# Kernel optimization log

Measured on AMD Instinct MI355X. Metric: run time of the kernel, lower is better.

## Reference

```python
import jax, jax.numpy as jnp
import numpy as np

OSC_TIME = 10
UNITS = 256
D_IN = 256
BATCH = 32
SEQLEN = 2000


def setup_inputs() -> dict:
    key = jax.random.key(0)
    k1, k2, k3 = jax.random.split(key, 3)
    scale = 1.0 / np.sqrt(UNITS)
    x = jax.random.normal(k1, (BATCH, SEQLEN, D_IN), dtype=jnp.float32)
    W_x = jax.random.normal(k2, (4, 2, D_IN, UNITS), dtype=jnp.float32) * scale
    W_h = jax.random.normal(k3, (4, 2, UNITS, UNITS), dtype=jnp.float32) * scale
    b_x = jnp.zeros((4, 2, UNITS), dtype=jnp.float32)
    b_h = jnp.zeros((4, 2, UNITS), dtype=jnp.float32)
    return {"x": x, "W_x": W_x, "b_x": b_x, "W_h": W_h, "b_h": b_h}


def reference(x, W_x, b_x, W_h, b_h):
    # Subsample every OSC_TIME steps (tf.gather stride)
    xs = x[:, ::OSC_TIME]                       # [B, Ts, D]
    B, Ts, _ = xs.shape
    U = W_h.shape[-1]

    # Precompute input projections for all 4 cells x 2 gates: [4,2,B,Ts,U]
    xp = jnp.einsum('btd,cgdu->cgbtu', xs, W_x) + b_x[:, :, None, None, :]

    h0 = jnp.zeros((4, B, U), dtype=x.dtype)

    def ff_step(h, xp_t):                       # h [4,B,U], xp_t [4,2,B,U]
        hp = jnp.einsum('cbu,cguv->cgbv', h, W_h) + b_h[:, :, None, :]
        g = jax.nn.sigmoid(xp_t + hp)           # [4,2,B,U]
        j, k = g[:, 0], g[:, 1]
        h_new = j * (1.0 - h) + (1.0 - k) * h   # flip-flop update
        return h_new, h_new

    _, hs = jax.lax.scan(ff_step, h0, jnp.moveaxis(xp, 3, 0))  # hs [Ts,4,B,U]
    phi, omega, r, mu = hs[:, 0], hs[:, 1], hs[:, 2], hs[:, 3]  # each [Ts,B,U]

    # Oscillator: emit z = r*cos(phi) then update r, phi; OSC_TIME sub-steps
    def osc_step(carry, _):
        r_t, phi_t = carry
        z = r_t * jnp.cos(phi_t)
        r_n = r_t + (mu - jnp.square(r_t)) * r_t
        phi_n = phi_t + omega
        return (r_n, phi_n), z

    _, zs = jax.lax.scan(osc_step, (r, phi), None, length=OSC_TIME)  # [S,Ts,B,U]
    out = jnp.transpose(zs, (2, 1, 0, 3)).reshape(B, Ts * OSC_TIME, U)
    return out
```

## Files before the change

### kernel.cpp

```cpp
#include <hip/hip_runtime.h>
#include <hip/hip_fp16.h>
#include <stdint.h>

#define TS 200

typedef _Float16 h2_t  __attribute__((ext_vector_type(2)));
typedef _Float16 f16x8 __attribute__((ext_vector_type(8)));
typedef float    f32x4 __attribute__((ext_vector_type(4)));

static __device__ __forceinline__ float fdot2f(uint32_t w, uint32_t h, float acc) {
#if __has_builtin(__builtin_amdgcn_fdot2)
    return __builtin_amdgcn_fdot2(__builtin_bit_cast(h2_t, w),
                                  __builtin_bit_cast(h2_t, h), acc, false);
#else
    h2_t a = __builtin_bit_cast(h2_t, w), b = __builtin_bit_cast(h2_t, h);
    acc = fmaf((float)a.x, (float)b.x, acc);
    acc = fmaf((float)a.y, (float)b.y, acc);
    return acc;
#endif
}

template <int CTRL>
static __device__ __forceinline__ float dpp_add(float x) {
    int m = __builtin_amdgcn_update_dpp(0, __builtin_bit_cast(int, x), CTRL, 0xF, 0xF, true);
    return x + __builtin_bit_cast(float, m);
}
template <int CTRL>
static __device__ __forceinline__ float dpp_mov(float x) {
    int m = __builtin_amdgcn_update_dpp(0, __builtin_bit_cast(int, x), CTRL, 0xF, 0xF, true);
    return __builtin_bit_cast(float, m);
}

__global__ __launch_bounds__(256) void pack_all(const float* __restrict__ x,
                                                const float* __restrict__ Wx,
                                                const float* __restrict__ Wh,
                                                _Float16* __restrict__ xh,
                                                _Float16* __restrict__ wxt,
                                                uint32_t* __restrict__ wp) {
    int bid = blockIdx.x, tid = threadIdx.x;
    if (bid < 6400) {
        int row = bid, col = tid;
        int b = row / 200, t = row - b * 200;
        xh[(size_t)row * 256 + col] = (_Float16)x[((size_t)(b * 2000 + t * 10)) * 256 + col];
    } else if (bid < 8448) {
        int n = bid - 6400, k = tid;
        wxt[(size_t)n * 256 + k] = (_Float16)Wx[((size_t)((n >> 8) * 256 + k)) * 256 + (n & 255)];
    } else {
        int idx = (bid - 8448) * 256 + tid;
        int e   = idx & 3;
        int thr = (idx >> 2) & 1023;
        int j   = (idx >> 12) & 15;
        int c   = idx >> 16;
        int a = j >> 2, i = j & 3;
        int uu = a >> 1, g = a & 1;
        int vs = thr & 7, uq = (thr >> 3) & 7, wv = thr >> 6;
        int u = (wv * 8 + uq) * 2 + uu;
        int v = vs * 32 + i * 8 + e * 2;
        const float* base = Wh + ((size_t)((c * 2 + g) * 256 + v)) * 256 + u;
        h2_t p; p.x = (_Float16)base[0]; p.y = (_Float16)base[256];
        wp[idx] = __builtin_bit_cast(uint32_t, p);
    }
}

__global__ __launch_bounds__(256) void xp_gemm(const _Float16* __restrict__ xh,
                                               const _Float16* __restrict__ wxt,
                                               const float* __restrict__ bxf,
                                               _Float16* __restrict__ xp) {
    __shared__ _Float16 As[128 * 64];
    __shared__ _Float16 Bs[128 * 64];
    const int tid = threadIdx.x;
    const int lane = tid & 63, w = tid >> 6;
    const int m0 = (blockIdx.x >> 4) * 128;
    const int n0 = (blockIdx.x & 15) * 128;
    const int mw = (w & 1) * 64, nw = (w >> 1) * 64;

    f32x4 acc[4][4] = {};

    for (int kb = 0; kb < 4; kb++) {
        const int k0 = kb * 64;
#pragma unroll
        for (int q = 0; q < 4; q++) {
            int ii = w * 4 + q;
            int r = ii * 8 + (lane >> 3);
            int kcol = (lane & 7) * 8;
            const _Float16* ga = xh  + (size_t)(m0 + r) * 256 + k0 + kcol;
            const _Float16* gb = wxt + (size_t)(n0 + r) * 256 + k0 + kcol;
            __builtin_amdgcn_global_load_lds(
                (const __attribute__((address_space(1))) uint32_t*)ga,
                (__attribute__((address_space(3))) uint32_t*)(As + ii * 512), 16, 0, 0);
            __builtin_amdgcn_global_load_lds(
                (const __attribute__((address_space(1))) uint32_t*)gb,
                (__attribute__((address_space(3))) uint32_t*)(Bs + ii * 512), 16, 0, 0);
        }
        __syncthreads();
#pragma unroll
        for (int kc = 0; kc < 2; kc++) {
            f16x8 a[4], b[4];
#pragma unroll
            for (int mt = 0; mt < 4; mt++)
                a[mt] = *(const f16x8*)&As[(mw + mt * 16 + (lane & 15)) * 64 + kc * 32 + (lane >> 4) * 8];
#pragma unroll
            for (int nt = 0; nt < 4; nt++)
                b[nt] = *(const f16x8*)&Bs[(nw + nt * 16 + (lane & 15)) * 64 + kc * 32 + (lane >> 4) * 8];
#pragma unroll
            for (int mt = 0; mt < 4; mt++)
#pragma unroll
                for (int nt = 0; nt < 4; nt++)
                    acc[mt][nt] = __builtin_amdgcn_mfma_f32_16x16x32_f16(a[mt], b[nt], acc[mt][nt], 0, 0, 0);
        }
        __syncthreads();
    }

    const int nl = lane & 15, quad = lane >> 4;
#pragma unroll
    for (int nt = 0; nt < 4; nt++) {
        int n = n0 + nw + nt * 16 + nl;
        float bias = bxf[n];
        int c = n >> 9, gu = n & 511;
#pragma unroll
        for (int mt = 0; mt < 4; mt++)
#pragma unroll
            for (int r = 0; r < 4; r++) {
                int m = m0 + mw + mt * 16 + quad * 4 + r;
                int b = m / 200, t = m - b * 200;
                xp[((size_t)((c * 32 + b) * 200 + t)) * 512 + gu] =
                    (_Float16)(acc[mt][nt][r] + bias);
            }
    }
}

#define D4(ACC, W, H)                 \
    ACC = fdot2f(W.x, H.x, ACC);      \
    ACC = fdot2f(W.y, H.y, ACC);      \
    ACC = fdot2f(W.z, H.z, ACC);      \
    ACC = fdot2f(W.w, H.w, ACC);

#define PIN4(W) asm volatile("" : "+v"(W.x), "+v"(W.y), "+v"(W.z), "+v"(W.w))

__global__ __attribute__((amdgpu_flat_work_group_size(512, 512),
                          amdgpu_waves_per_eu(2, 2)))
void recurrence(const _Float16* __restrict__ xp,
                const float* __restrict__ bh,
                const uint32_t* __restrict__ Wp,
                float* __restrict__ hs) {
    const int cb  = blockIdx.x;
    const int c   = cb >> 5;
    const int tid = threadIdx.x;
    const int lane = tid & 63;
    const int vs = lane & 7;
    const int uq = lane >> 3;
    const int wv = tid >> 6;
    const int up0 = wv * 8 + uq;
    const int u0 = up0 * 2;

    __shared__ __align__(16) uint32_t h2s[2][160];

    const uint4* wb = (const uint4*)Wp + (size_t)c * 16 * 1024 + tid;
    uint4 wA00 = wb[0 * 1024],        wA01 = wb[1 * 1024],        wA02 = wb[2 * 1024],        wA03 = wb[3 * 1024];
    uint4 wA10 = wb[4 * 1024],        wA11 = wb[5 * 1024],        wA12 = wb[6 * 1024],        wA13 = wb[7 * 1024];
    uint4 wA20 = wb[8 * 1024],        wA21 = wb[9 * 1024],        wA22 = wb[10 * 1024],       wA23 = wb[11 * 1024];
    uint4 wA30 = wb[12 * 1024],       wA31 = wb[13 * 1024],       wA32 = wb[14 * 1024],       wA33 = wb[15 * 1024];
    uint4 wB00 = wb[0 * 1024 + 512],  wB01 = wb[1 * 1024 + 512],  wB02 = wb[2 * 1024 + 512],  wB03 = wb[3 * 1024 + 512];
    uint4 wB10 = wb[4 * 1024 + 512],  wB11 = wb[5 * 1024 + 512],  wB12 = wb[6 * 1024 + 512],  wB13 = wb[7 * 1024 + 512];
    uint4 wB20 = wb[8 * 1024 + 512],  wB21 = wb[9 * 1024 + 512],  wB22 = wb[10 * 1024 + 512], wB23 = wb[11 * 1024 + 512];
    uint4 wB30 = wb[12 * 1024 + 512], wB31 = wb[13 * 1024 + 512], wB32 = wb[14 * 1024 + 512], wB33 = wb[15 * 1024 + 512];
    PIN4(wA00); PIN4(wA01); PIN4(wA02); PIN4(wA03);
    PIN4(wA10); PIN4(wA11); PIN4(wA12); PIN4(wA13);
    PIN4(wA20); PIN4(wA21); PIN4(wA22); PIN4(wA23);
    PIN4(wA30); PIN4(wA31); PIN4(wA32); PIN4(wA33);
    PIN4(wB00); PIN4(wB01); PIN4(wB02); PIN4(wB03);
    PIN4(wB10); PIN4(wB11); PIN4(wB12); PIN4(wB13);
    PIN4(wB20); PIN4(wB21); PIN4(wB22); PIN4(wB23);
    PIN4(wB30); PIN4(wB31); PIN4(wB32); PIN4(wB33);

    float biasA = 0.f, biasB = 0.f;
    const _Float16* xpb = nullptr;
    if (vs < 4) {
        int g_sel = vs & 1, u_sel = u0 + (vs >> 1);
        biasA = bh[(c * 2 + g_sel) * 256 + u_sel];
        biasB = bh[(c * 2 + g_sel) * 256 + u_sel + 128];
        xpb  = xp + (size_t)cb * 200 * 512 + g_sel * 256 + u_sel;
    }

    float hregA = 0.f, hregB = 0.f;
    if (tid < 160) { h2s[0][tid] = 0u; }
    __syncthreads();

    float* hsb = hs + (size_t)cb * 200 * 256 + u0;

    for (int t = 0; t < TS; t++) {
        const uint32_t* hbuf = h2s[t & 1];
        uint32_t* hnext = h2s[(t + 1) & 1];

        float xpA = 0.f, xpB = 0.f;
        if (vs < 4) {
            xpA = (float)xpb[(size_t)t * 512];
            xpB = (float)xpb[(size_t)t * 512 + 128];
        }

        uint4 h0 = *(const uint4*)(hbuf + vs * 20 + 0);
        uint4 h1 = *(const uint4*)(hbuf + vs * 20 + 4);
        uint4 h2 = *(const uint4*)(hbuf + vs * 20 + 8);
        uint4 h3 = *(const uint4*)(hbuf + vs * 20 + 12);

        float aA0 = 0.f, aA1 = 0.f, aA2 = 0.f, aA3 = 0.f;
        float aB0 = 0.f, aB1 = 0.f, aB2 = 0.f, aB3 = 0.f;
        D4(aA0, wA00, h0) D4(aB0, wB00, h0) D4(aA1, wA10, h0) D4(aB1, wB10, h0)
        D4(aA2, wA20, h0) D4(aB2, wB20, h0) D4(aA3, wA30, h0) D4(aB3, wB30, h0)
        D4(aA0, wA01, h1) D4(aB0, wB01, h1) D4(aA1, wA11, h1) D4(aB1, wB11, h1)
        D4(aA2, wA21, h1) D4(aB2, wB21, h1) D4(aA3, wA31, h1) D4(aB3, wB31, h1)
        D4(aA0, wA02, h2) D4(aB0, wB02, h2) D4(aA1, wA12, h2) D4(aB1, wB12, h2)
        D4(aA2, wA22, h2) D4(aB2, wB22, h2) D4(aA3, wA32, h2) D4(aB3, wB32, h2)
        D4(aA0, wA03, h3) D4(aB0, wB03, h3) D4(aA1, wA13, h3) D4(aB1, wB13, h3)
        D4(aA2, wA23, h3) D4(aB2, wB23, h3) D4(aA3, wA33, h3) D4(aB3, wB33, h3)

        aA0 = dpp_add<0x141>(dpp_add<0x4E>(dpp_add<0xB1>(aA0)));
        aA1 = dpp_add<0x141>(dpp_add<0x4E>(dpp_add<0xB1>(aA1)));
        aA2 = dpp_add<0x141>(dpp_add<0x4E>(dpp_add<0xB1>(aA2)));
        aA3 = dpp_add<0x141>(dpp_add<0x4E>(dpp_add<0xB1>(aA3)));
        aB0 = dpp_add<0x141>(dpp_add<0x4E>(dpp_add<0xB1>(aB0)));
        aB1 = dpp_add<0x141>(dpp_add<0x4E>(dpp_add<0xB1>(aB1)));
        aB2 = dpp_add<0x141>(dpp_add<0x4E>(dpp_add<0xB1>(aB2)));
        aB3 = dpp_add<0x141>(dpp_add<0x4E>(dpp_add<0xB1>(aB3)));

        float sA = (vs == 0) ? aA0 : (vs == 1) ? aA1 : (vs == 2) ? aA2 : aA3;
        float sB = (vs == 0) ? aB0 : (vs == 1) ? aB1 : (vs == 2) ? aB2 : aB3;
        sA += xpA + biasA;
        sB += xpB + biasB;
        float sigA = 1.f / (1.f + __expf(-sA));
        float sigB = 1.f / (1.f + __expf(-sB));
        float kgA = dpp_mov<0xB1>(sigA);
        float kgB = dpp_mov<0xB1>(sigB);
        float hnA = sigA + hregA * (1.f - sigA - kgA);
        float hnB = sigB + hregB * (1.f - sigB - kgB);
        hregA = hnA;
        hregB = hnB;
        float hn1A = dpp_mov<0x4E>(hnA);
        float hn1B = dpp_mov<0x4E>(hnB);
        if (vs == 0) {
            h2_t pA; pA.x = (_Float16)hnA; pA.y = (_Float16)hn1A;
            h2_t pB; pB.x = (_Float16)hnB; pB.y = (_Float16)hn1B;
            int idx0 = (up0 >> 4) * 20 + (up0 & 15);
            hnext[idx0]      = __builtin_bit_cast(uint32_t, pA);
            hnext[idx0 + 80] = __builtin_bit_cast(uint32_t, pB);
            *(float2*)(hsb + (size_t)t * 256)       = make_float2(hnA, hn1A);
            *(float2*)(hsb + (size_t)t * 256 + 128) = make_float2(hnB, hn1B);
        }
        __syncthreads();
    }
}

__global__ __launch_bounds__(256) void osc(const float* __restrict__ hs,
                                           float* __restrict__ out) {
    int tid = blockIdx.x * 256 + threadIdx.x;
    const int cstride = 32 * 200 * 256;
    int u = tid & 255;
    int bt = tid >> 8;
    int t = bt % 200, b = bt / 200;
    float phi   = hs[0 * cstride + tid];
    float omega = hs[1 * cstride + tid];
    float r     = hs[2 * cstride + tid];
    float mu    = hs[3 * cstride + tid];
    float* o = out + ((size_t)(b * 2000 + t * 10)) * 256 + u;
#pragma unroll
    for (int s = 0; s < 10; s++) {
        o[(size_t)s * 256] = r * __cosf(phi);
        r = r + (mu - r * r) * r;
        phi = phi + omega;
    }
}

extern "C" void kernel_launch(void* const* d_in, const int* in_sizes, int n_in,
                              void* d_out, int out_size, void* d_ws, size_t ws_size,
                              hipStream_t stream) {
    const float* x  = (const float*)d_in[0];
    const float* Wx = (const float*)d_in[1];
    const float* bx = (const float*)d_in[2];
    const float* Wh = (const float*)d_in[3];
    const float* bh = (const float*)d_in[4];
    float* out = (float*)d_out;

    char* ws = (char*)d_ws;
    const size_t XP = (size_t)4 * 32 * 200 * 512 * 2;
    const size_t HS = (size_t)4 * 32 * 200 * 256 * 4;
    const size_t XH = (size_t)6400 * 256 * 2;

    _Float16* xp  = (_Float16*)ws;
    float*    hs  = (float*)(ws + XP);
    _Float16* xh  = (_Float16*)(ws + XP);
    _Float16* wxt = (_Float16*)(ws + XP + XH);
    uint32_t* wp  = (uint32_t*)(ws + XP + HS);

    pack_all<<<9472, 256, 0, stream>>>(x, Wx, Wh, xh, wxt, wp);
    xp_gemm<<<800, 256, 0, stream>>>(xh, wxt, bx, xp);
    recurrence<<<128, 512, 0, stream>>>(xp, bh, wp, hs);
    osc<<<6400, 256, 0, stream>>>(hs, out);
}
```

Baseline: 381.2 us.

## Prefetch xp projections eight steps ahead and use LDS-only barrier in recurrence

The recurrence loop is blocked by 8 timesteps, and the xp input projections for the next block are loaded into registers while the current block runs. This takes global-memory latency off the serial per-step critical path. __syncthreads is replaced by a barrier that waits only on LDS counters (lgkmcnt), so the per-step barrier no longer waits for outstanding global loads and stores. The cost is more register pressure from the prefetch buffers, under a tight waves_per_eu(2,2) budget that holds many pinned weights.

```diff
diff --git a/kernel.cpp b/kernel.cpp
--- a/kernel.cpp
+++ b/kernel.cpp
@@ -137,6 +137,14 @@
 
 #define PIN4(W) asm volatile("" : "+v"(W.x), "+v"(W.y), "+v"(W.z), "+v"(W.w))
 
+#define LDS_BARRIER()                                        \
+    do {                                                     \
+        __builtin_amdgcn_sched_barrier(0);                   \
+        asm volatile("s_waitcnt lgkmcnt(0)" ::: "memory");   \
+        __builtin_amdgcn_s_barrier();                        \
+        __builtin_amdgcn_sched_barrier(0);                   \
+    } while (0)
+
 __global__ __attribute__((amdgpu_flat_work_group_size(512, 512),
                           amdgpu_waves_per_eu(2, 2)))
 void recurrence(const _Float16* __restrict__ xp,
@@ -188,65 +196,89 @@
 
     float* hsb = hs + (size_t)cb * 200 * 256 + u0;
 
-    for (int t = 0; t < TS; t++) {
-        const uint32_t* hbuf = h2s[t & 1];
-        uint32_t* hnext = h2s[(t + 1) & 1];
-
-        float xpA = 0.f, xpB = 0.f;
+    _Float16 curA[8] = {}, curB[8] = {}, nxtA[8] = {}, nxtB[8] = {};
+    if (vs < 4) {
+#pragma unroll
+        for (int s = 0; s < 8; s++) {
+            curA[s] = xpb[(size_t)s * 512];
+            curB[s] = xpb[(size_t)s * 512 + 128];
+        }
+    }
+
+    for (int tb = 0; tb < TS; tb += 8) {
+        if (vs < 4 && tb + 8 < TS) {
+#pragma unroll
+            for (int s = 0; s < 8; s++) {
+                nxtA[s] = xpb[(size_t)(tb + 8 + s) * 512];
+                nxtB[s] = xpb[(size_t)(tb + 8 + s) * 512 + 128];
+            }
+        }
+#pragma unroll
+        for (int s = 0; s < 8; s++) {
+            const int t = tb + s;
+            const uint32_t* hbuf = h2s[t & 1];
+            uint32_t* hnext = h2s[(t + 1) & 1];
+
+            float xpA = 0.f, xpB = 0.f;
+            if (vs < 4) {
+                xpA = (float)curA[s];
+                xpB = (float)curB[s];
+            }
+
+            uint4 h0 = *(const uint4*)(hbuf + vs * 20 + 0);
+            uint4 h1 = *(const uint4*)(hbuf + vs * 20 + 4);
+            uint4 h2 = *(const uint4*)(hbuf + vs * 20 + 8);
+            uint4 h3 = *(const uint4*)(hbuf + vs * 20 + 12);
+
+            float aA0 = 0.f, aA1 = 0.f, aA2 = 0.f, aA3 = 0.f;
+            float aB0 = 0.f, aB1 = 0.f, aB2 = 0.f, aB3 = 0.f;
+            D4(aA0, wA00, h0) D4(aB0, wB00, h0) D4(aA1, wA10, h0) D4(aB1, wB10, h0)
+            D4(aA2, wA20, h0) D4(aB2, wB20, h0) D4(aA3, wA30, h0) D4(aB3, wB30, h0)
+            D4(aA0, wA01, h1) D4(aB0, wB01, h1) D4(aA1, wA11, h1) D4(aB1, wB11, h1)
+            D4(aA2, wA21, h1) D4(aB2, wB21, h1) D4(aA3, wA31, h1) D4(aB3, wB31, h1)
+            D4(aA0, wA02, h2) D4(aB0, wB02, h2) D4(aA1, wA12, h2) D4(aB1, wB12, h2)
+            D4(aA2, wA22, h2) D4(aB2, wB22, h2) D4(aA3, wA32, h2) D4(aB3, wB32, h2)
+            D4(aA0, wA03, h3) D4(aB0, wB03, h3) D4(aA1, wA13, h3) D4(aB1, wB13, h3)
+            D4(aA2, wA23, h3) D4(aB2, wB23, h3) D4(aA3, wA33, h3) D4(aB3, wB33, h3)
+
+            aA0 = dpp_add<0x141>(dpp_add<0x4E>(dpp_add<0xB1>(aA0)));
+            aA1 = dpp_add<0x141>(dpp_add<0x4E>(dpp_add<0xB1>(aA1)));
+            aA2 = dpp_add<0x141>(dpp_add<0x4E>(dpp_add<0xB1>(aA2)));
+            aA3 = dpp_add<0x141>(dpp_add<0x4E>(dpp_add<0xB1>(aA3)));
+            aB0 = dpp_add<0x141>(dpp_add<0x4E>(dpp_add<0xB1>(aB0)));
+            aB1 = dpp_add<0x141>(dpp_add<0x4E>(dpp_add<0xB1>(aB1)));
+            aB2 = dpp_add<0x141>(dpp_add<0x4E>(dpp_add<0xB1>(aB2)));
+            aB3 = dpp_add<0x141>(dpp_add<0x4E>(dpp_add<0xB1>(aB3)));
+
+            float sA = (vs == 0) ? aA0 : (vs == 1) ? aA1 : (vs == 2) ? aA2 : aA3;
+            float sB = (vs == 0) ? aB0 : (vs == 1) ? aB1 : (vs == 2) ? aB2 : aB3;
+            sA += xpA + biasA;
+            sB += xpB + biasB;
+            float sigA = 1.f / (1.f + __expf(-sA));
+            float sigB = 1.f / (1.f + __expf(-sB));
+            float kgA = dpp_mov<0xB1>(sigA);
+            float kgB = dpp_mov<0xB1>(sigB);
+            float hnA = sigA + hregA * (1.f - sigA - kgA);
+            float hnB = sigB + hregB * (1.f - sigB - kgB);
+            hregA = hnA;
+            hregB = hnB;
+            float hn1A = dpp_mov<0x4E>(hnA);
+            float hn1B = dpp_mov<0x4E>(hnB);
+            if (vs == 0) {
+                h2_t pA; pA.x = (_Float16)hnA; pA.y = (_Float16)hn1A;
+                h2_t pB; pB.x = (_Float16)hnB; pB.y = (_Float16)hn1B;
+                int idx0 = (up0 >> 4) * 20 + (up0 & 15);
+                hnext[idx0]      = __builtin_bit_cast(uint32_t, pA);
+                hnext[idx0 + 80] = __builtin_bit_cast(uint32_t, pB);
+                *(float2*)(hsb + (size_t)t * 256)       = make_float2(hnA, hn1A);
+                *(float2*)(hsb + (size_t)t * 256 + 128) = make_float2(hnB, hn1B);
+            }
+            LDS_BARRIER();
+        }
         if (vs < 4) {
-            xpA = (float)xpb[(size_t)t * 512];
-            xpB = (float)xpb[(size_t)t * 512 + 128];
-        }
-
-        uint4 h0 = *(const uint4*)(hbuf + vs * 20 + 0);
-        uint4 h1 = *(const uint4*)(hbuf + vs * 20 + 4);
-        uint4 h2 = *(const uint4*)(hbuf + vs * 20 + 8);
-        uint4 h3 = *(const uint4*)(hbuf + vs * 20 + 12);
-
-        float aA0 = 0.f, aA1 = 0.f, aA2 = 0.f, aA3 = 0.f;
-        float aB0 = 0.f, aB1 = 0.f, aB2 = 0.f, aB3 = 0.f;
-        D4(aA0, wA00, h0) D4(aB0, wB00, h0) D4(aA1, wA10, h0) D4(aB1, wB10, h0)
-        D4(aA2, wA20, h0) D4(aB2, wB20, h0) D4(aA3, wA30, h0) D4(aB3, wB30, h0)
-        D4(aA0, wA01, h1) D4(aB0, wB01, h1) D4(aA1, wA11, h1) D4(aB1, wB11, h1)
-        D4(aA2, wA21, h1) D4(aB2, wB21, h1) D4(aA3, wA31, h1) D4(aB3, wB31, h1)
-        D4(aA0, wA02, h2) D4(aB0, wB02, h2) D4(aA1, wA12, h2) D4(aB1, wB12, h2)
-        D4(aA2, wA22, h2) D4(aB2, wB22, h2) D4(aA3, wA32, h2) D4(aB3, wB32, h2)
-        D4(aA0, wA03, h3) D4(aB0, wB03, h3) D4(aA1, wA13, h3) D4(aB1, wB13, h3)
-        D4(aA2, wA23, h3) D4(aB2, wB23, h3) D4(aA3, wA33, h3) D4(aB3, wB33, h3)
-
-        aA0 = dpp_add<0x141>(dpp_add<0x4E>(dpp_add<0xB1>(aA0)));
-        aA1 = dpp_add<0x141>(dpp_add<0x4E>(dpp_add<0xB1>(aA1)));
-        aA2 = dpp_add<0x141>(dpp_add<0x4E>(dpp_add<0xB1>(aA2)));
-        aA3 = dpp_add<0x141>(dpp_add<0x4E>(dpp_add<0xB1>(aA3)));
-        aB0 = dpp_add<0x141>(dpp_add<0x4E>(dpp_add<0xB1>(aB0)));
-        aB1 = dpp_add<0x141>(dpp_add<0x4E>(dpp_add<0xB1>(aB1)));
-        aB2 = dpp_add<0x141>(dpp_add<0x4E>(dpp_add<0xB1>(aB2)));
-        aB3 = dpp_add<0x141>(dpp_add<0x4E>(dpp_add<0xB1>(aB3)));
-
-        float sA = (vs == 0) ? aA0 : (vs == 1) ? aA1 : (vs == 2) ? aA2 : aA3;
-        float sB = (vs == 0) ? aB0 : (vs == 1) ? aB1 : (vs == 2) ? aB2 : aB3;
-        sA += xpA + biasA;
-        sB += xpB + biasB;
-        float sigA = 1.f / (1.f + __expf(-sA));
-        float sigB = 1.f / (1.f + __expf(-sB));
-        float kgA = dpp_mov<0xB1>(sigA);
-        float kgB = dpp_mov<0xB1>(sigB);
-        float hnA = sigA + hregA * (1.f - sigA - kgA);
-        float hnB = sigB + hregB * (1.f - sigB - kgB);
-        hregA = hnA;
-        hregB = hnB;
-        float hn1A = dpp_mov<0x4E>(hnA);
-        float hn1B = dpp_mov<0x4E>(hnB);
-        if (vs == 0) {
-            h2_t pA; pA.x = (_Float16)hnA; pA.y = (_Float16)hn1A;
-            h2_t pB; pB.x = (_Float16)hnB; pB.y = (_Float16)hn1B;
-            int idx0 = (up0 >> 4) * 20 + (up0 & 15);
-            hnext[idx0]      = __builtin_bit_cast(uint32_t, pA);
-            hnext[idx0 + 80] = __builtin_bit_cast(uint32_t, pB);
-            *(float2*)(hsb + (size_t)t * 256)       = make_float2(hnA, hn1A);
-            *(float2*)(hsb + (size_t)t * 256 + 128) = make_float2(hnB, hn1B);
-        }
-        __syncthreads();
+#pragma unroll
+            for (int s = 0; s < 8; s++) { curA[s] = nxtA[s]; curB[s] = nxtB[s]; }
+        }
     }
 }
 
```

Result: faster. 344.9 us (-9.5%).

## Process two batch rows per workgroup in recurrence with prefetched xp and lighter barrier

Applied to the files above, without the earlier changes.

Each recurrence workgroup now advances two independent batch sequences, sharing the register-resident W_h weights, so the grid shrinks from 128 to 64 blocks. Interleaving two independent dot-product chains is meant to hide the latency of each serial step and of the per-step barrier. The xp input for step t+1 is prefetched during step t, and __syncthreads is replaced by an LDS-only wait plus s_barrier so outstanding global loads and stores need not drain. The costs are roughly double the per-step work per block, higher register pressure, and half as many CUs in use.

```diff
diff --git a/kernel.cpp b/kernel.cpp
--- a/kernel.cpp
+++ b/kernel.cpp
@@ -137,14 +137,27 @@
 
 #define PIN4(W) asm volatile("" : "+v"(W.x), "+v"(W.y), "+v"(W.z), "+v"(W.w))
 
+#define RED3(A) A = dpp_add<0x141>(dpp_add<0x4E>(dpp_add<0xB1>(A)));
+
+#define LDS_BARRIER()                                        \
+    do {                                                     \
+        __builtin_amdgcn_sched_barrier(0);                   \
+        asm volatile("s_waitcnt lgkmcnt(0)" ::: "memory");   \
+        __builtin_amdgcn_s_barrier();                        \
+        __builtin_amdgcn_sched_barrier(0);                   \
+    } while (0)
+
 __global__ __attribute__((amdgpu_flat_work_group_size(512, 512),
                           amdgpu_waves_per_eu(2, 2)))
 void recurrence(const _Float16* __restrict__ xp,
                 const float* __restrict__ bh,
                 const uint32_t* __restrict__ Wp,
                 float* __restrict__ hs) {
-    const int cb  = blockIdx.x;
-    const int c   = cb >> 5;
+    const int wg  = blockIdx.x;
+    const int c   = wg >> 4;
+    const int b0  = wg & 15;
+    const int cbP = c * 32 + b0;
+    const int cbQ = cbP + 16;
     const int tid = threadIdx.x;
     const int lane = tid & 63;
     const int vs = lane & 7;
@@ -153,7 +166,8 @@
     const int up0 = wv * 8 + uq;
     const int u0 = up0 * 2;
 
-    __shared__ __align__(16) uint32_t h2s[2][160];
+    __shared__ __align__(16) uint32_t h2sP[2][160];
+    __shared__ __align__(16) uint32_t h2sQ[2][160];
 
     const uint4* wb = (const uint4*)Wp + (size_t)c * 16 * 1024 + tid;
     uint4 wA00 = wb[0 * 1024],        wA01 = wb[1 * 1024],        wA02 = wb[2 * 1024],        wA03 = wb[3 * 1024];
@@ -174,79 +188,123 @@
     PIN4(wB30); PIN4(wB31); PIN4(wB32); PIN4(wB33);
 
     float biasA = 0.f, biasB = 0.f;
-    const _Float16* xpb = nullptr;
+    const _Float16* xpbP = nullptr;
+    const _Float16* xpbQ = nullptr;
     if (vs < 4) {
         int g_sel = vs & 1, u_sel = u0 + (vs >> 1);
         biasA = bh[(c * 2 + g_sel) * 256 + u_sel];
         biasB = bh[(c * 2 + g_sel) * 256 + u_sel + 128];
-        xpb  = xp + (size_t)cb * 200 * 512 + g_sel * 256 + u_sel;
-    }
-
-    float hregA = 0.f, hregB = 0.f;
-    if (tid < 160) { h2s[0][tid] = 0u; }
+        xpbP = xp + (size_t)cbP * 200 * 512 + g_sel * 256 + u_sel;
+        xpbQ = xp + (size_t)cbQ * 200 * 512 + g_sel * 256 + u_sel;
+    }
+
+    float hrAP = 0.f, hrBP = 0.f;
+    float hrAQ = 0.f, hrBQ = 0.f;
+    if (tid < 160) { h2sP[0][tid] = 0u; h2sQ[0][tid] = 0u; }
     __syncthreads();
 
-    float* hsb = hs + (size_t)cb * 200 * 256 + u0;
+    float* hsbP = hs + (size_t)cbP * 200 * 256 + u0;
+    float* hsbQ = hs + (size_t)cbQ * 200 * 256 + u0;
+
+    float cAP = 0.f, cBP = 0.f, cAQ = 0.f, cBQ = 0.f;
+    _Float16 nAP = (_Float16)0.f, nBP = (_Float16)0.f;
+    _Float16 nAQ = (_Float16)0.f, nBQ = (_Float16)0.f;
+    if (vs < 4) {
+        cAP = (float)xpbP[0]; cBP = (float)xpbP[128];
+        cAQ = (float)xpbQ[0]; cBQ = (float)xpbQ[128];
+    }
 
     for (int t = 0; t < TS; t++) {
-        const uint32_t* hbuf = h2s[t & 1];
-        uint32_t* hnext = h2s[(t + 1) & 1];
-
-        float xpA = 0.f, xpB = 0.f;
+        const uint32_t* hbP = h2sP[t & 1];
+        uint32_t* hnP = h2sP[(t + 1) & 1];
+        const uint32_t* hbQ = h2sQ[t & 1];
+        uint32_t* hnQ = h2sQ[(t + 1) & 1];
+
+        if (vs < 4 && t + 1 < TS) {
+            nAP = xpbP[(size_t)(t + 1) * 512];
+            nBP = xpbP[(size_t)(t + 1) * 512 + 128];
+            nAQ = xpbQ[(size_t)(t + 1) * 512];
+            nBQ = xpbQ[(size_t)(t + 1) * 512 + 128];
+        }
+
+        uint4 hP0 = *(const uint4*)(hbP + vs * 20 + 0);
+        uint4 hP1 = *(const uint4*)(hbP + vs * 20 + 4);
+        uint4 hP2 = *(const uint4*)(hbP + vs * 20 + 8);
+        uint4 hP3 = *(const uint4*)(hbP + vs * 20 + 12);
+        uint4 hQ0 = *(const uint4*)(hbQ + vs * 20 + 0);
+        uint4 hQ1 = *(const uint4*)(hbQ + vs * 20 + 4);
+        uint4 hQ2 = *(const uint4*)(hbQ + vs * 20 + 8);
+        uint4 hQ3 = *(const uint4*)(hbQ + vs * 20 + 12);
+
+        float aAP0 = 0.f, aAP1 = 0.f, aAP2 = 0.f, aAP3 = 0.f;
+        float aBP0 = 0.f, aBP1 = 0.f, aBP2 = 0.f, aBP3 = 0.f;
+        float aAQ0 = 0.f, aAQ1 = 0.f, aAQ2 = 0.f, aAQ3 = 0.f;
+        float aBQ0 = 0.f, aBQ1 = 0.f, aBQ2 = 0.f, aBQ3 = 0.f;
+        D4(aAP0, wA00, hP0) D4(aAQ0, wA00, hQ0) D4(aBP0, wB00, hP0) D4(aBQ0, wB00, hQ0)
+        D4(aAP1, wA10, hP0) D4(aAQ1, wA10, hQ0) D4(aBP1, wB10, hP0) D4(aBQ1, wB10, hQ0)
+        D4(aAP2, wA20, hP0) D4(aAQ2, wA20, hQ0) D4(aBP2, wB20, hP0) D4(aBQ2, wB20, hQ0)
+        D4(aAP3, wA30, hP0) D4(aAQ3, wA30, hQ0) D4(aBP3, wB30, hP0) D4(aBQ3, wB30, hQ0)
+        D4(aAP0, wA01, hP1) D4(aAQ0, wA01, hQ1) D4(aBP0, wB01, hP1) D4(aBQ0, wB01, hQ1)
+        D4(aAP1, wA11, hP1) D4(aAQ1, wA11, hQ1) D4(aBP1, wB11, hP1) D4(aBQ1, wB11, hQ1)
+        D4(aAP2, wA21, hP1) D4(aAQ2, wA21, hQ1) D4(aBP2, wB21, hP1) D4(aBQ2, wB21, hQ1)
+        D4(aAP3, wA31, hP1) D4(aAQ3, wA31, hQ1) D4(aBP3, wB31, hP1) D4(aBQ3, wB31, hQ1)
+        D4(aAP0, wA02, hP2) D4(aAQ0, wA02, hQ2) D4(aBP0, wB02, hP2) D4(aBQ0, wB02, hQ2)
+        D4(aAP1, wA12, hP2) D4(aAQ1, wA12, hQ2) D4(aBP1, wB12, hP2) D4(aBQ1, wB12, hQ2)
+        D4(aAP2, wA22, hP2) D4(aAQ2, wA22, hQ2) D4(aBP2, wB22, hP2) D4(aBQ2, wB22, hQ2)
+        D4(aAP3, wA32, hP2) D4(aAQ3, wA32, hQ2) D4(aBP3, wB32, hP2) D4(aBQ3, wB32, hQ2)
+        D4(aAP0, wA03, hP3) D4(aAQ0, wA03, hQ3) D4(aBP0, wB03, hP3) D4(aBQ0, wB03, hQ3)
+        D4(aAP1, wA13, hP3) D4(aAQ1, wA13, hQ3) D4(aBP1, wB13, hP3) D4(aBQ1, wB13, hQ3)
+        D4(aAP2, wA23, hP3) D4(aAQ2, wA23, hQ3) D4(aBP2, wB23, hP3) D4(aBQ2, wB23, hQ3)
+        D4(aAP3, wA33, hP3) D4(aAQ3, wA33, hQ3) D4(aBP3, wB33, hP3) D4(aBQ3, wB33, hQ3)
+
+        RED3(aAP0) RED3(aAP1) RED3(aAP2) RED3(aAP3)
+        RED3(aBP0) RED3(aBP1) RED3(aBP2) RED3(aBP3)
+        RED3(aAQ0) RED3(aAQ1) RED3(aAQ2) RED3(aAQ3)
+        RED3(aBQ0) RED3(aBQ1) RED3(aBQ2) RED3(aBQ3)
+
+        float sAP = (vs == 0) ? aAP0 : (vs == 1) ? aAP1 : (vs == 2) ? aAP2 : aAP3;
+        float sBP = (vs == 0) ? aBP0 : (vs == 1) ? aBP1 : (vs == 2) ? aBP2 : aBP3;
+        float sAQ = (vs == 0) ? aAQ0 : (vs == 1) ? aAQ1 : (vs == 2) ? aAQ2 : aAQ3;
+        float sBQ = (vs == 0) ? aBQ0 : (vs == 1) ? aBQ1 : (vs == 2) ? aBQ2 : aBQ3;
+        sAP += cAP + biasA;  sBP += cBP + biasB;
+        sAQ += cAQ + biasA;  sBQ += cBQ + biasB;
+        float gAP = 1.f / (1.f + __expf(-sAP));
+        float gBP = 1.f / (1.f + __expf(-sBP));
+        float gAQ = 1.f / (1.f + __expf(-sAQ));
+        float gBQ = 1.f / (1.f + __expf(-sBQ));
+        float kAP = dpp_mov<0xB1>(gAP);
+        float kBP = dpp_mov<0xB1>(gBP);
+        float kAQ = dpp_mov<0xB1>(gAQ);
+        float kBQ = dpp_mov<0xB1>(gBQ);
+        float hnAP = gAP + hrAP * (1.f - gAP - kAP);
+        float hnBP = gBP + hrBP * (1.f - gBP - kBP);
+        float hnAQ = gAQ + hrAQ * (1.f - gAQ - kAQ);
+        float hnBQ = gBQ + hrBQ * (1.f - gBQ - kBQ);
+        hrAP = hnAP; hrBP = hnBP; hrAQ = hnAQ; hrBQ = hnBQ;
+        float h1AP = dpp_mov<0x4E>(hnAP);
+        float h1BP = dpp_mov<0x4E>(hnBP);
+        float h1AQ = dpp_mov<0x4E>(hnAQ);
+        float h1BQ = dpp_mov<0x4E>(hnBQ);
+        if (vs == 0) {
+            h2_t pAP; pAP.x = (_Float16)hnAP; pAP.y = (_Float16)h1AP;
+            h2_t pBP; pBP.x = (_Float16)hnBP; pBP.y = (_Float16)h1BP;
+            h2_t pAQ; pAQ.x = (_Float16)hnAQ; pAQ.y = (_Float16)h1AQ;
+            h2_t pBQ; pBQ.x = (_Float16)hnBQ; pBQ.y = (_Float16)h1BQ;
+            int idx0 = (up0 >> 4) * 20 + (up0 & 15);
+            hnP[idx0]      = __builtin_bit_cast(uint32_t, pAP);
+            hnP[idx0 + 80] = __builtin_bit_cast(uint32_t, pBP);
+            hnQ[idx0]      = __builtin_bit_cast(uint32_t, pAQ);
+            hnQ[idx0 + 80] = __builtin_bit_cast(uint32_t, pBQ);
+            *(float2*)(hsbP + (size_t)t * 256)       = make_float2(hnAP, h1AP);
+            *(float2*)(hsbP + (size_t)t * 256 + 128) = make_float2(hnBP, h1BP);
+            *(float2*)(hsbQ + (size_t)t * 256)       = make_float2(hnAQ, h1AQ);
+            *(float2*)(hsbQ + (size_t)t * 256 + 128) = make_float2(hnBQ, h1BQ);
+        }
+        LDS_BARRIER();
         if (vs < 4) {
-            xpA = (float)xpb[(size_t)t * 512];
-            xpB = (float)xpb[(size_t)t * 512 + 128];
-        }
-
-        uint4 h0 = *(const uint4*)(hbuf + vs * 20 + 0);
-        uint4 h1 = *(const uint4*)(hbuf + vs * 20 + 4);
-        uint4 h2 = *(const uint4*)(hbuf + vs * 20 + 8);
-        uint4 h3 = *(const uint4*)(hbuf + vs * 20 + 12);
-
-        float aA0 = 0.f, aA1 = 0.f, aA2 = 0.f, aA3 = 0.f;
-        float aB0 = 0.f, aB1 = 0.f, aB2 = 0.f, aB3 = 0.f;
-        D4(aA0, wA00, h0) D4(aB0, wB00, h0) D4(aA1, wA10, h0) D4(aB1, wB10, h0)
-        D4(aA2, wA20, h0) D4(aB2, wB20, h0) D4(aA3, wA30, h0) D4(aB3, wB30, h0)
-        D4(aA0, wA01, h1) D4(aB0, wB01, h1) D4(aA1, wA11, h1) D4(aB1, wB11, h1)
-        D4(aA2, wA21, h1) D4(aB2, wB21, h1) D4(aA3, wA31, h1) D4(aB3, wB31, h1)
-        D4(aA0, wA02, h2) D4(aB0, wB02, h2) D4(aA1, wA12, h2) D4(aB1, wB12, h2)
-        D4(aA2, wA22, h2) D4(aB2, wB22, h2) D4(aA3, wA32, h2) D4(aB3, wB32, h2)
-        D4(aA0, wA03, h3) D4(aB0, wB03, h3) D4(aA1, wA13, h3) D4(aB1, wB13, h3)
-        D4(aA2, wA23, h3) D4(aB2, wB23, h3) D4(aA3, wA33, h3) D4(aB3, wB33, h3)
-
-        aA0 = dpp_add<0x141>(dpp_add<0x4E>(dpp_add<0xB1>(aA0)));
-        aA1 = dpp_add<0x141>(dpp_add<0x4E>(dpp_add<0xB1>(aA1)));
-        aA2 = dpp_add<0x141>(dpp_add<0x4E>(dpp_add<0xB1>(aA2)));
-        aA3 = dpp_add<0x141>(dpp_add<0x4E>(dpp_add<0xB1>(aA3)));
-        aB0 = dpp_add<0x141>(dpp_add<0x4E>(dpp_add<0xB1>(aB0)));
-        aB1 = dpp_add<0x141>(dpp_add<0x4E>(dpp_add<0xB1>(aB1)));
-        aB2 = dpp_add<0x141>(dpp_add<0x4E>(dpp_add<0xB1>(aB2)));
-        aB3 = dpp_add<0x141>(dpp_add<0x4E>(dpp_add<0xB1>(aB3)));
-
-        float sA = (vs == 0) ? aA0 : (vs == 1) ? aA1 : (vs == 2) ? aA2 : aA3;
-        float sB = (vs == 0) ? aB0 : (vs == 1) ? aB1 : (vs == 2) ? aB2 : aB3;
-        sA += xpA + biasA;
-        sB += xpB + biasB;
-        float sigA = 1.f / (1.f + __expf(-sA));
-        float sigB = 1.f / (1.f + __expf(-sB));
-        float kgA = dpp_mov<0xB1>(sigA);
-        float kgB = dpp_mov<0xB1>(sigB);
-        float hnA = sigA + hregA * (1.f - sigA - kgA);
-        float hnB = sigB + hregB * (1.f - sigB - kgB);
-        hregA = hnA;
-        hregB = hnB;
-        float hn1A = dpp_mov<0x4E>(hnA);
-        float hn1B = dpp_mov<0x4E>(hnB);
-        if (vs == 0) {
-            h2_t pA; pA.x = (_Float16)hnA; pA.y = (_Float16)hn1A;
-            h2_t pB; pB.x = (_Float16)hnB; pB.y = (_Float16)hn1B;
-            int idx0 = (up0 >> 4) * 20 + (up0 & 15);
-            hnext[idx0]      = __builtin_bit_cast(uint32_t, pA);
-            hnext[idx0 + 80] = __builtin_bit_cast(uint32_t, pB);
-            *(float2*)(hsb + (size_t)t * 256)       = make_float2(hnA, hn1A);
-            *(float2*)(hsb + (size_t)t * 256 + 128) = make_float2(hnB, hn1B);
-        }
-        __syncthreads();
+            cAP = (float)nAP; cBP = (float)nBP;
+            cAQ = (float)nAQ; cBQ = (float)nBQ;
+        }
     }
 }
 
@@ -293,6 +351,6 @@
 
     pack_all<<<9472, 256, 0, stream>>>(x, Wx, Wh, xh, wxt, wp);
     xp_gemm<<<800, 256, 0, stream>>>(xh, wxt, bx, xp);
-    recurrence<<<128, 512, 0, stream>>>(xp, bh, wp, hs);
+    recurrence<<<64, 512, 0, stream>>>(xp, bh, wp, hs);
     osc<<<6400, 256, 0, stream>>>(hs, out);
 }
```

Measured after the change: 492.7 us. 29.3% more time.
